# Kernel optimization log

Hardware: AMD Instinct MI355X
Metric: run time of the kernel (lower is better)

Reference implementation:

```python
import jax, jax.numpy as jnp
import numpy as np

N = 2_097_152
D = 128
B = 8192


def setup_inputs() -> dict:
    key = jax.random.key(0)
    k1, k2 = jax.random.split(key)
    atom_features = jax.random.normal(k1, (N, D), dtype=jnp.float32)
    segment_ids = jnp.sort(jax.random.randint(k2, (N,), 0, B, dtype=jnp.int64))
    return {
        "atom_features": atom_features,
        "segment_ids": segment_ids,
        "num_segments": B,
    }


def reference(atom_features, segment_ids, num_segments):
    # Segment mean: per-crystal average of atom features.
    # Equivalent to the original per-group jnp.mean gather loop, fused into
    # a single scatter-add + count pass.
    sums = jax.ops.segment_sum(atom_features, segment_ids, num_segments=num_segments)
    counts = jax.ops.segment_sum(
        jnp.ones((atom_features.shape[0],), dtype=atom_features.dtype),
        segment_ids,
        num_segments=num_segments,
    )
    # guard against empty segments (original assumes every group non-empty)
    return sums / jnp.maximum(counts, 1.0)[:, None]
```

## Files before the change

kernel.cpp:

```cpp
#include <hip/hip_runtime.h>

#define FEAT_D 128
#define TPB 256
#define ROWGROUPS (TPB / 32)

__global__ __launch_bounds__(TPB) void seg_mean_kernel(
    const float* __restrict__ feat,
    const int* __restrict__ ids,
    float* __restrict__ out,
    int N)
{
    const int s = blockIdx.x;

    __shared__ int s_bounds[2];
    if (threadIdx.x < 2) {
        const int target = s + (int)threadIdx.x;
        int lo = 0, hi = N;
        while (lo < hi) {
            int mid = (lo + hi) >> 1;
            if (ids[mid] < target) lo = mid + 1; else hi = mid;
        }
        s_bounds[threadIdx.x] = lo;
    }
    __syncthreads();
    const int start = s_bounds[0];
    const int end   = s_bounds[1];
    const int cnt   = end - start;

    const int col4 = threadIdx.x & 31;
    const int rg   = threadIdx.x >> 5;
    const float4* fp = (const float4*)feat;

    float4 acc = make_float4(0.f, 0.f, 0.f, 0.f);
    for (int r = start + rg; r < end; r += ROWGROUPS) {
        float4 v = fp[(size_t)r * 32 + col4];
        acc.x += v.x; acc.y += v.y; acc.z += v.z; acc.w += v.w;
    }

    __shared__ float4 red[ROWGROUPS][32];
    red[rg][col4] = acc;
    __syncthreads();

    if (rg == 0) {
        float4 t = red[0][col4];
        #pragma unroll
        for (int g = 1; g < ROWGROUPS; ++g) {
            float4 u = red[g][col4];
            t.x += u.x; t.y += u.y; t.z += u.z; t.w += u.w;
        }
        const float inv = 1.0f / (float)max(cnt, 1);
        t.x *= inv; t.y *= inv; t.z *= inv; t.w *= inv;
        ((float4*)out)[(size_t)s * 32 + col4] = t;
    }
}

extern "C" void kernel_launch(void* const* d_in, const int* in_sizes, int n_in,
                              void* d_out, int out_size, void* d_ws, size_t ws_size,
                              hipStream_t stream) {
    const float* feat = (const float*)d_in[0];
    const int*   ids  = (const int*)d_in[1];
    float*       out  = (float*)d_out;

    const int N = in_sizes[0] / FEAT_D;
    const int B = out_size / FEAT_D;

    seg_mean_kernel<<<B, TPB, 0, stream>>>(feat, ids, out, N);
}
```

Measured before the change: 206.5 us.

## Use wave-parallel 64-ary segment search and per-wave contiguous row streaming

Replaces the single-thread binary search for segment bounds with a wave-wide 64-ary search that uses ballot, cutting the serial chain of dependent global loads. Each wave now streams a contiguous slice of the segment's rows with two accumulators and nontemporal loads, instead of rows interleaved across the whole block. The per-wave halves are combined with a cross-lane shuffle before a smaller shared-memory reduction. This adds more complex indexing in exchange for shorter search latency and more loads in flight.

```diff
diff --git a/kernel.cpp b/kernel.cpp
--- a/kernel.cpp
+++ b/kernel.cpp
@@ -1,8 +1,11 @@
 #include <hip/hip_runtime.h>
 
 #define FEAT_D 128
-#define TPB 256
-#define ROWGROUPS (TPB / 32)
+#define D4     32
+#define TPB    256
+#define NWAVES 4
+
+typedef float f32x4 __attribute__((ext_vector_type(4)));
 
 __global__ __launch_bounds__(TPB) void seg_mean_kernel(
     const float* __restrict__ feat,
@@ -10,47 +13,85 @@
     float* __restrict__ out,
     int N)
 {
-    const int s = blockIdx.x;
+    const int s    = blockIdx.x;
+    const int tid  = (int)threadIdx.x;
+    const int lane = tid & 63;
+    const int wave = tid >> 6;
 
     __shared__ int s_bounds[2];
-    if (threadIdx.x < 2) {
-        const int target = s + (int)threadIdx.x;
+    if (wave < 2) {
+        const int target = s + wave;
         int lo = 0, hi = N;
-        while (lo < hi) {
-            int mid = (lo + hi) >> 1;
-            if (ids[mid] < target) lo = mid + 1; else hi = mid;
+        while (hi - lo > 64) {
+            const unsigned span = (unsigned)(hi - lo);
+            const int p  = lo + (int)(((unsigned long long)span * (unsigned)lane) >> 6);
+            const bool c = (ids[p] < target);
+            const unsigned long long m = __ballot(c);
+            if (m == 0ull) { hi = lo; break; }
+            const int h = 63 - __builtin_clzll(m);
+            const int ph  = lo + (int)(((unsigned long long)span * (unsigned)h) >> 6);
+            const int ph1 = (h < 63)
+                ? lo + (int)(((unsigned long long)span * (unsigned)(h + 1)) >> 6)
+                : hi;
+            lo = ph + 1;
+            hi = ph1;
         }
-        s_bounds[threadIdx.x] = lo;
+        const int idx = lo + lane;
+        const bool c  = (idx < hi) && (ids[idx] < target);
+        const int cnt = __popcll(__ballot(c));
+        if (lane == 0) s_bounds[wave] = lo + cnt;
     }
     __syncthreads();
+
     const int start = s_bounds[0];
     const int end   = s_bounds[1];
     const int cnt   = end - start;
 
-    const int col4 = threadIdx.x & 31;
-    const int rg   = threadIdx.x >> 5;
-    const float4* fp = (const float4*)feat;
+    const int q    = cnt >> 2;
+    const int rem  = cnt & 3;
+    const int wbeg = start + q * wave + min(wave, rem);
+    const int wcnt = q + (wave < rem ? 1 : 0);
+    const int wend = wbeg + wcnt;
 
-    float4 acc = make_float4(0.f, 0.f, 0.f, 0.f);
-    for (int r = start + rg; r < end; r += ROWGROUPS) {
-        float4 v = fp[(size_t)r * 32 + col4];
-        acc.x += v.x; acc.y += v.y; acc.z += v.z; acc.w += v.w;
+    const int rpar = lane >> 5;
+    const int col4 = lane & 31;
+    const f32x4* fp = (const f32x4*)feat + col4;
+
+    f32x4 a0 = (f32x4)(0.f);
+    f32x4 a1 = (f32x4)(0.f);
+
+    int r = wbeg + rpar;
+    for (; r + 2 < wend; r += 4) {
+        const f32x4 v0 = __builtin_nontemporal_load(&fp[(size_t)r       * D4]);
+        const f32x4 v1 = __builtin_nontemporal_load(&fp[(size_t)(r + 2) * D4]);
+        a0 += v0;
+        a1 += v1;
     }
+    for (; r < wend; r += 2) {
+        a0 += __builtin_nontemporal_load(&fp[(size_t)r * D4]);
+    }
+    a0 += a1;
 
-    __shared__ float4 red[ROWGROUPS][32];
-    red[rg][col4] = acc;
+    f32x4 o;
+    o.x = __shfl_xor(a0.x, 32);
+    o.y = __shfl_xor(a0.y, 32);
+    o.z = __shfl_xor(a0.z, 32);
+    o.w = __shfl_xor(a0.w, 32);
+    a0 += o;
+
+    __shared__ f32x4 red[NWAVES][D4];
+    if ((lane >> 5) == 0) red[wave][col4] = a0;
     __syncthreads();
 
-    if (rg == 0) {
-        float4 t = red[0][col4];
+    if (tid < D4) {
+        f32x4 t = red[0][tid];
         #pragma unroll
-        for (int g = 1; g < ROWGROUPS; ++g) {
-            float4 u = red[g][col4];
-            t.x += u.x; t.y += u.y; t.z += u.z; t.w += u.w;
+        for (int g = 1; g < NWAVES; ++g) {
+            t += red[g][tid];
         }
         const float inv = 1.0f / (float)max(cnt, 1);
-        t.x *= inv; t.y *= inv; t.z *= inv; t.w *= inv;
-        ((float4*)out)[(size_t)s * 32 + col4] = t;
+        t *= inv;
+        ((f32x4*)out)[(size_t)s * D4 + tid] = t;
     }
 }
 
```

New measurement: 174.7 us. 15.4% less time.
